# Performance work log

Hardware: AMD Instinct MI355X
Metric: run time of the kernel (lower is better)

## Reference

```python
import jax, jax.numpy as jnp
import numpy as np

T, B, D, H, L = 512, 128, 400, 400, 3


def setup_inputs() -> dict:
    key = jax.random.key(0)
    ks = jax.random.split(key, 12)
    x = jax.random.normal(ks[0], (T, B, D), dtype=jnp.float32)
    lengths = jnp.sort(jax.random.randint(ks[1], (B,), 1, T + 1))[::-1]
    s = 1.0 / np.sqrt(H)
    def w(k, shape):
        return jax.random.normal(k, shape, dtype=jnp.float32) * s
    return {
        "x": x,
        "lengths": lengths,
        # forward-direction cells: layer0 input D, layers 1..2 input 2H
        "Wih_f0": w(ks[2], (4 * H, D)),
        "Wih_f12": w(ks[3], (L - 1, 4 * H, 2 * H)),
        "Whh_f": w(ks[4], (L, 4 * H, H)),
        "b_f": jnp.zeros((L, 4 * H), jnp.float32),
        # backward-direction cells
        "Wih_b0": w(ks[5], (4 * H, D)),
        "Wih_b12": w(ks[6], (L - 1, 4 * H, 2 * H)),
        "Whh_b": w(ks[7], (L, 4 * H, H)),
        "b_b": jnp.zeros((L, 4 * H), jnp.float32),
    }


def _layer(x, mask, Wih, Whh, bias, reverse):
    # x: [T,B,Din], mask: [T,B] bool. Precompute input-side gates once.
    gx = jnp.einsum("tbd,gd->tbg", x, Wih) + bias  # [T,B,4H]
    nb, h_dim = x.shape[1], Whh.shape[-1]

    def step(carry, inp):
        h, c = carry
        g_x, m = inp
        g = g_x + h @ Whh.T
        i, f, gc, o = jnp.split(g, 4, axis=-1)
        i, f, o = jax.nn.sigmoid(i), jax.nn.sigmoid(f), jax.nn.sigmoid(o)
        gc = jnp.tanh(gc)
        c_new = f * c + i * gc
        h_new = o * jnp.tanh(c_new)
        m = m[:, None]
        # inactive sequences keep old state (fwd) / init zeros (bwd) -- matches packed semantics
        h = jnp.where(m, h_new, h)
        c = jnp.where(m, c_new, c)
        return (h, c), h

    if reverse:
        gx, m_seq = gx[::-1], mask[::-1]
    else:
        m_seq = mask
    init = (jnp.zeros((nb, h_dim), x.dtype), jnp.zeros((nb, h_dim), x.dtype))
    _, out = jax.lax.scan(step, init, (gx, m_seq))
    if reverse:
        out = out[::-1]
    return out * mask[:, :, None]


def reference(x, lengths, Wih_f0, Wih_f12, Whh_f, b_f, Wih_b0, Wih_b12, Whh_b, b_b):
    mask = jnp.arange(x.shape[0])[:, None] < lengths[None, :]  # [T,B]
    Wih_fs = [Wih_f0, Wih_f12[0], Wih_f12[1]]
    Wih_bs = [Wih_b0, Wih_b12[0], Wih_b12[1]]
    for l in range(L):
        f = _layer(x, mask, Wih_fs[l], Whh_f[l], b_f[l], reverse=False)
        b = _layer(x, mask, Wih_bs[l], Whh_b[l], b_b[l], reverse=True)
        x = jnp.concatenate([f, b], axis=-1)  # [T,B,2H]
    return x
```

## Files before the change

### kernel.cpp

```cpp
#include <hip/hip_runtime.h>
#include <stdint.h>
#include <stddef.h>

#define T_ 512
#define B_ 128
#define D_ 400
#define H_ 400
#define HP 416
#define GP 1664
#define NW 3328
#define K0P 448
#define K12P 832
#define NTILES 13
#define NGRP 8
#define REC_BLOCKS 208
#define PAIRS 208

#define GC_FSTRIDE 576

#define HBT_U64   ((size_t)16*2*16*PAIRS)
#define HBT_BYTES (HBT_U64*8)

#define WHHR_US8  ((size_t)2*13*4*2*13*64)
#define WHHR_BYTES (WHHR_US8*8*2)

typedef __attribute__((ext_vector_type(8))) __bf16 bf16x8;
typedef __attribute__((ext_vector_type(4))) float f32x4;
typedef __attribute__((ext_vector_type(8))) unsigned short us8;

__device__ __forceinline__ unsigned short f2bf(float f){
  unsigned u = __builtin_bit_cast(unsigned, f);
  u = (u + 0x7FFFu + ((u >> 16) & 1u)) >> 16;
  return (unsigned short)u;
}
__device__ __forceinline__ float bf2f(unsigned short s){
  unsigned u = ((unsigned)s) << 16;
  return __builtin_bit_cast(float, u);
}
__device__ __forceinline__ float sigm(float x){ return 1.f / (1.f + __expf(-x)); }
__device__ __forceinline__ float tanh_f(float x){
  float ax = fabsf(x);
  float e = __expf(-2.f * ax);
  float t = (1.f - e) / (1.f + e);
  return x < 0.f ? -t : t;
}
__device__ __forceinline__ void store_gx(float* p, float v){ *p = v; }
__device__ __forceinline__ void store_gx(unsigned short* p, float v){ *p = f2bf(v); }

__device__ __forceinline__ void h_store_u64(unsigned long long* p, unsigned long long v){
  __hip_atomic_store(p, v, __ATOMIC_RELAXED, __HIP_MEMORY_SCOPE_AGENT);
}
__device__ __forceinline__ unsigned long long h_load_u64(const unsigned long long* p){
  return __hip_atomic_load(p, __ATOMIC_RELAXED, __HIP_MEMORY_SCOPE_AGENT);
}

__device__ __forceinline__ void gl_lds16(const unsigned short* g, unsigned short* l){
  __builtin_amdgcn_global_load_lds(
      (const __attribute__((address_space(1))) unsigned int*)g,
      (__attribute__((address_space(3))) unsigned int*)l, 16, 0, 0);
}

__global__ void k_conv_x0(const float* __restrict__ x, unsigned short* __restrict__ xa){
  const size_t i = (size_t)blockIdx.x*256 + threadIdx.x;
  if (i >= (size_t)T_*B_*K0P) return;
  const int k = (int)(i % K0P);
  const size_t tb = i / K0P;
  xa[i] = f2bf(k < D_ ? x[tb*D_ + k] : 0.f);
}

__global__ void k_prep_wih(const float* __restrict__ wf, const float* __restrict__ wb,
                           int K, int mode, unsigned short* __restrict__ dst){
  const size_t i = (size_t)blockIdx.x*256 + threadIdx.x;
  if (i >= (size_t)NW*K) return;
  const int k = (int)(i % K);
  const int n = (int)(i / K);
  const int d = n / GP, ng = n % GP, g = ng / HP, r = ng % HP;
  const float* Wsrc = d ? wb : wf;
  float v = 0.f;
  if (r < H_){
    if (mode == 0){
      if (k < D_) v = Wsrc[(size_t)(g*H_ + r)*D_ + k];
    } else {
      int ks = (k < 400) ? k : ((k >= 416 && k < 816) ? (k - 16) : -1);
      if (ks >= 0) v = Wsrc[(size_t)(g*H_ + r)*800 + ks];
    }
  }
  dst[i] = f2bf(v);
}

__global__ void k_prep_whhR(const float* __restrict__ wf, const float* __restrict__ wb,
                            unsigned short* __restrict__ dst){
  const size_t i = (size_t)blockIdx.x*256 + threadIdx.x;
  if (i >= WHHR_US8) return;
  const int lane = (int)(i & 63);
  size_t q = i >> 6;
  const int kk = (int)(q % 13); q /= 13;
  const int ch = (int)(q % 2);  q /= 2;
  const int w  = (int)(q % 4);  q /= 4;
  const int tile = (int)(q % 13);
  const int dirx = (int)(q / 13);
  const int c  = tile*32 + ch*16 + (lane & 15);
  const int k0 = kk*32 + (lane >> 4)*8;
  const float* W = dirx ? wb : wf;
  unsigned short v[8];
  #pragma unroll
  for (int e = 0; e < 8; ++e){
    const int k = k0 + e;
    const float x = (c < H_ && k < H_) ? W[(size_t)(w*H_ + c)*H_ + k] : 0.f;
    v[e] = f2bf(x);
  }
  *(us8*)(dst + i*8) = *(const us8*)v;
}

__global__ void k_prep_bias(const float* __restrict__ bsf, const float* __restrict__ bsb,
                            float* __restrict__ dst){
  const int n = blockIdx.x*256 + threadIdx.x;
  if (n >= NW) return;
  const int d = n / GP, ng = n % GP, g = ng / HP, r = ng % HP;
  dst[n] = (r < H_) ? (d ? bsb : bsf)[g*H_ + r] : 0.f;
}

template<typename GXT>
__global__ __launch_bounds__(256) void gemm_gx(
    const unsigned short* __restrict__ X, int lda, int K,
    const unsigned short* __restrict__ W,
    const float* __restrict__ bias,
    GXT* __restrict__ gx,
    const int* __restrict__ lens)
{
  const int t = blockIdx.y;
  if (t >= lens[0]) return;
  const int n0 = blockIdx.x * 128;
  __shared__ unsigned short As[128*64];
  __shared__ unsigned short Bs[128*64];
  const int tid = threadIdx.x;
  const int l = tid & 63;
  const int w = tid >> 6;
  const int wm = (w >> 1) * 64, wn = (w & 1) * 64;
  const int lr = l & 15, lk = l >> 4;
  f32x4 acc[4][4];
  #pragma unroll
  for (int i = 0; i < 4; ++i)
    #pragma unroll
    for (int j = 0; j < 4; ++j) acc[i][j] = (f32x4){0.f,0.f,0.f,0.f};

  const unsigned short* Xb = X + (size_t)t * B_ * lda;
  const int srow = l >> 3, scol = (l & 7) * 8;

  for (int k0 = 0; k0 < K; k0 += 64){
    #pragma unroll
    for (int c = 0; c < 4; ++c){
      const int rb = w*32 + c*8;
      gl_lds16(Xb + (size_t)(rb + srow)*lda + k0 + scol, &As[rb*64]);
      gl_lds16(W  + (size_t)(n0 + rb + srow)*K  + k0 + scol, &Bs[rb*64]);
    }
    __syncthreads();
    #pragma unroll
    for (int kk = 0; kk < 2; ++kk){
      bf16x8 af[4], bfr[4];
      #pragma unroll
      for (int mi = 0; mi < 4; ++mi)
        af[mi] = __builtin_bit_cast(bf16x8, *(const us8*)&As[(wm + mi*16 + lr)*64 + kk*32 + lk*8]);
      #pragma unroll
      for (int ni = 0; ni < 4; ++ni)
        bfr[ni] = __builtin_bit_cast(bf16x8, *(const us8*)&Bs[(wn + ni*16 + lr)*64 + kk*32 + lk*8]);
      #pragma unroll
      for (int mi = 0; mi < 4; ++mi)
        #pragma unroll
        for (int ni = 0; ni < 4; ++ni)
          acc[mi][ni] = __builtin_amdgcn_mfma_f32_16x16x32_bf16(af[mi], bfr[ni], acc[mi][ni], 0, 0, 0);
    }
    __syncthreads();
  }
  #pragma unroll
  for (int ni = 0; ni < 4; ++ni){
    const int col = n0 + wn + ni*16 + lr;
    const float bv = bias[col];
    #pragma unroll
    for (int mi = 0; mi < 4; ++mi){
      #pragma unroll
      for (int r = 0; r < 4; ++r){
        const int b = wm + mi*16 + lk*4 + r;
        store_gx(gx + ((size_t)t*B_ + b)*NW + col, acc[mi][ni][r] + bv);
      }
    }
  }
}

template<typename GXT, bool LAST>
__global__ __launch_bounds__(256, 1) void lstm_rec(
    const GXT* __restrict__ gx,
    const unsigned short* __restrict__ whhR,
    const int* __restrict__ lens,
    unsigned long long* hbt,
    unsigned short* __restrict__ xn,
    float* __restrict__ out)
{
  __shared__ unsigned short HS[16*424];
  __shared__ float GC[4*GC_FSTRIDE];
  __shared__ float GXS[16*132];

  const int tid = threadIdx.x;
  const int bid = blockIdx.x;
  const int dir  = bid / 104;
  const int rem  = bid % 104;
  const int grp  = rem / NTILES;
  const int tile = rem % NTILES;
  const int l  = tid & 63;
  const int w  = tid >> 6;
  const int lr = l & 15;
  const int lk = l >> 4;
  const int cid = dir*NGRP + grp;

  us8 Bf0[13], Bf1[13];
  {
    const unsigned short* bs =
        whhR + ((size_t)((dir*13 + tile)*4 + w)*2*13*64 + l)*8;
    #pragma unroll
    for (int kk = 0; kk < 13; ++kk)
      Bf0[kk] = *(const us8*)(bs + (size_t)kk*512);
    const unsigned short* bs1 = bs + (size_t)13*64*8;
    #pragma unroll
    for (int kk = 0; kk < 13; ++kk)
      Bf1[kk] = *(const us8*)(bs1 + (size_t)kk*512);
  }
  const int grp_len = lens[grp*16];
  const int eb  = tid & 15;
  const int p2  = tid >> 4;
  const int mylen = lens[grp*16 + eb];
  float cs0 = 0.f, cs1 = 0.f, hs0 = 0.f, hs1 = 0.f;
  __syncthreads();

  int s_a = 0;
  const int pb = tid >> 4, q = tid & 15, qg = q >> 2, qj = (q & 3) * 8;
  unsigned long long* const myslot =
      hbt + (((size_t)cid*2)*16 + eb)*PAIRS + tile*16 + p2;

  for (int s = 0; s < T_; ++s){
    const int t = dir ? (T_ - 1 - s) : s;
    if (t >= grp_len) continue;

    f32x4 pfa, pfb;
    {
      const size_t goff = ((size_t)t*B_ + grp*16 + pb) * NW + (size_t)dir*GP + qg*HP + tile*32 + qj;
      if constexpr (sizeof(GXT) == 4){
        const float* gp = (const float*)gx + goff;
        pfa = *(const f32x4*)gp;
        pfb = *(const f32x4*)(gp + 4);
      } else {
        us8 v = *(const us8*)((const unsigned short*)gx + goff);
        pfa = (f32x4){bf2f(v[0]), bf2f(v[1]), bf2f(v[2]), bf2f(v[3])};
        pfb = (f32x4){bf2f(v[4]), bf2f(v[5]), bf2f(v[6]), bf2f(v[7])};
      }
    }

    {
      const unsigned rtag = (unsigned)s_a;
      const unsigned long long* hb =
          hbt + ((size_t)(cid*2 + (s_a & 1))*16)*PAIRS;
      unsigned long long v[13];
      #pragma unroll
      for (int j = 0; j < 13; ++j)
        v[j] = h_load_u64(hb + j*256 + tid);
      unsigned stale = 0;
      #pragma unroll
      for (int j = 0; j < 13; ++j)
        if ((unsigned)(v[j] >> 32) != rtag) stale |= 1u << j;
      while (stale){
        const unsigned m = stale;
        #pragma unroll
        for (int j = 0; j < 13; ++j)
          if (m & (1u << j)) v[j] = h_load_u64(hb + j*256 + tid);
        #pragma unroll
        for (int j = 0; j < 13; ++j)
          if ((m & (1u << j)) && (unsigned)(v[j] >> 32) == rtag) stale &= ~(1u << j);
      }
      #pragma unroll
      for (int j = 0; j < 13; ++j){
        const int idx = j*256 + tid;
        const int b = idx / PAIRS, p = idx % PAIRS;
        *(unsigned*)&HS[b*424 + 2*p] = (unsigned)v[j];
      }
    }
    __syncthreads();

    f32x4 a0 = (f32x4){0.f,0.f,0.f,0.f}, a1 = (f32x4){0.f,0.f,0.f,0.f};
    {
      const int ab = lr*424 + lk*8;
      #pragma unroll
      for (int kk = 0; kk < 13; ++kk){
        bf16x8 av = __builtin_bit_cast(bf16x8, *(const us8*)&HS[ab + kk*32]);
        a0 = __builtin_amdgcn_mfma_f32_16x16x32_bf16(av, Bf0[kk], a0, 0, 0, 0);
        a1 = __builtin_amdgcn_mfma_f32_16x16x32_bf16(av, Bf1[kk], a1, 0, 0, 0);
      }
    }
    {
      float* Gw = GC + w * GC_FSTRIDE;
      #pragma unroll
      for (int r = 0; r < 4; ++r){
        Gw[(lk*4 + r)*36 + lr]      = a0[r];
        Gw[(lk*4 + r)*36 + 16 + lr] = a1[r];
      }
      float* gp = GXS + pb*132 + qg*32 + qj;
      *(f32x4*)gp = pfa;
      *(f32x4*)(gp + 4) = pfb;
    }
    __syncthreads();

    const bool act = t < mylen;
    const int c0 = 2*p2, c1 = 2*p2 + 1;
    {
      const float gi0 = GC[0*GC_FSTRIDE + eb*36 + c0] + GXS[eb*132 + c0];
      const float gf0 = GC[1*GC_FSTRIDE + eb*36 + c0] + GXS[eb*132 + 32 + c0];
      const float gg0 = GC[2*GC_FSTRIDE + eb*36 + c0] + GXS[eb*132 + 64 + c0];
      const float go0 = GC[3*GC_FSTRIDE + eb*36 + c0] + GXS[eb*132 + 96 + c0];
      const float gi1 = GC[0*GC_FSTRIDE + eb*36 + c1] + GXS[eb*132 + c1];
      const float gf1 = GC[1*GC_FSTRIDE + eb*36 + c1] + GXS[eb*132 + 32 + c1];
      const float gg1 = GC[2*GC_FSTRIDE + eb*36 + c1] + GXS[eb*132 + 64 + c1];
      const float go1 = GC[3*GC_FSTRIDE + eb*36 + c1] + GXS[eb*132 + 96 + c1];
      const float cn0 = sigm(gf0)*cs0 + sigm(gi0)*tanh_f(gg0);
      const float hn0 = sigm(go0) * tanh_f(cn0);
      const float cn1 = sigm(gf1)*cs1 + sigm(gi1)*tanh_f(gg1);
      const float hn1 = sigm(go1) * tanh_f(cn1);
      if (act){ cs0 = cn0; hs0 = hn0; cs1 = cn1; hs1 = hn1; }
    }
    {
      const unsigned hu = (unsigned)f2bf(hs0) | ((unsigned)f2bf(hs1) << 16);
      const unsigned long long hv =
          (unsigned long long)hu | ((unsigned long long)(unsigned)(s_a + 1) << 32);
      h_store_u64(myslot + ((size_t)((s_a + 1) & 1))*16*PAIRS, hv);
    }
    if (act){
      const int bg = grp*16 + eb;
      const int hc = tile*32 + c0;
      if constexpr (LAST){
        float* op = out + ((size_t)t*B_ + bg)*800 + dir*H_ + hc;
        if (hc < H_)     op[0] = hs0;
        if (hc + 1 < H_) op[1] = hs1;
      } else {
        const unsigned hu = (unsigned)f2bf(hs0) | ((unsigned)f2bf(hs1) << 16);
        *(unsigned*)(xn + ((size_t)t*B_ + bg)*832 + (size_t)dir*HP + hc) = hu;
      }
    }
    ++s_a;
  }
}

template<typename GXT>
static void run_all(void* const* din, float* out, char* ws, hipStream_t stream)
{
  const float* x      = (const float*)din[0];
  const int* lens     = (const int*)din[1];
  const float* wihf0  = (const float*)din[2];
  const float* wihf12 = (const float*)din[3];
  const float* whhf   = (const float*)din[4];
  const float* bsf    = (const float*)din[5];
  const float* wihb0  = (const float*)din[6];
  const float* wihb12 = (const float*)din[7];
  const float* whhb   = (const float*)din[8];
  const float* bsb    = (const float*)din[9];

  char* p = ws;
  auto alloc = [&](size_t n){ char* r = p; p += (n + 255) & ~(size_t)255; return r; };
  GXT* gx            = (GXT*)alloc((size_t)T_*B_*NW*sizeof(GXT));
  unsigned short* xA = (unsigned short*)alloc((size_t)T_*B_*832*2);
  unsigned short* xB = (unsigned short*)alloc((size_t)T_*B_*832*2);
  unsigned short* wihp = (unsigned short*)alloc((size_t)NW*K12P*2);
  unsigned short* whhR = (unsigned short*)alloc(WHHR_BYTES);
  float* biasp       = (float*)alloc((size_t)NW*4);
  unsigned long long* hbt = (unsigned long long*)alloc(HBT_BYTES);

  hipMemsetAsync(out, 0, (size_t)T_*B_*800*4, stream);
  {
    size_t n = (size_t)T_*B_*K0P;
    k_conv_x0<<<dim3((unsigned)((n+255)/256)), dim3(256), 0, stream>>>(x, xA);
  }

  const unsigned short* xin[3] = {xA, xB, xA};
  unsigned short* xout[3] = {xB, xA, nullptr};
  const int ldas[3] = {K0P, 832, 832};
  const int Ks[3]   = {K0P, K12P, K12P};

  for (int lyr = 0; lyr < 3; ++lyr){
    const float* wf = (lyr == 0) ? wihf0 : wihf12 + (size_t)(lyr-1)*1600*800;
    const float* wb = (lyr == 0) ? wihb0 : wihb12 + (size_t)(lyr-1)*1600*800;
    {
      size_t n = (size_t)NW*Ks[lyr];
      k_prep_wih<<<dim3((unsigned)((n+255)/256)), dim3(256), 0, stream>>>(
          wf, wb, Ks[lyr], lyr ? 1 : 0, wihp);
    }
    k_prep_bias<<<dim3((NW+255)/256), dim3(256), 0, stream>>>(
        bsf + (size_t)lyr*1600, bsb + (size_t)lyr*1600, biasp);
    gemm_gx<GXT><<<dim3(26, 512), dim3(256), 0, stream>>>(
        xin[lyr], ldas[lyr], Ks[lyr], wihp, biasp, gx, lens);
    {
      size_t n = WHHR_US8;
      k_prep_whhR<<<dim3((unsigned)((n+255)/256)), dim3(256), 0, stream>>>(
          whhf + (size_t)lyr*1600*400, whhb + (size_t)lyr*1600*400, whhR);
    }
    hipMemsetAsync(hbt, 0, HBT_BYTES, stream);

    if (lyr < 2)
      lstm_rec<GXT,false><<<dim3(REC_BLOCKS), dim3(256), 0, stream>>>(
          gx, whhR, lens, hbt, xout[lyr], out);
    else
      lstm_rec<GXT,true><<<dim3(REC_BLOCKS), dim3(256), 0, stream>>>(
          gx, whhR, lens, hbt, nullptr, out);
  }
}

extern "C" void kernel_launch(void* const* d_in, const int* in_sizes, int n_in,
                              void* d_out, int out_size, void* d_ws, size_t ws_size,
                              hipStream_t stream)
{
  (void)in_sizes; (void)n_in; (void)out_size;
  auto align = [](size_t n){ return (n + 255) & ~(size_t)255; };
  const size_t fixed =
      align((size_t)T_*B_*832*2) * 2 +
      align((size_t)NW*K12P*2) +
      align(WHHR_BYTES) +
      align((size_t)NW*4) +
      align(HBT_BYTES);
  const size_t need32 = align((size_t)T_*B_*NW*4) + fixed;
  const size_t need16 = align((size_t)T_*B_*NW*2) + fixed;

  if (ws_size >= need32)
    run_all<float>(d_in, (float*)d_out, (char*)d_ws, stream);
  else if (ws_size >= need16)
    run_all<unsigned short>(d_in, (float*)d_out, (char*)d_ws, stream);
  else
    hipMemsetAsync(d_out, 0, (size_t)T_*B_*800*4, stream);
}
```

Measured before the change: 6.327 ms.

## Fuse input-projection GEMM into recurrent LSTM kernel with register-resident Wih

Removes the separate gx GEMM and its large T*B*4H intermediate buffer. Each recurrent block now keeps its slice of Wih in registers (26 k-chunks per gate pair), stages the x row for the current timestep into LDS, and does the input projection with MFMA inside every step before adding the recurrent term. The aim is to cut the gx write/read traffic and the extra launch. In exchange, the serial critical path of each step now carries twice the MFMA work plus an x load, and register pressure rises sharply (52 extra us8 fragments), which risks spills. Layer 0 input is also padded to 832 columns.

```diff
diff --git a/kernel.cpp b/kernel.cpp
--- a/kernel.cpp
+++ b/kernel.cpp
@@ -9,8 +9,7 @@
 #define HP 416
 #define GP 1664
 #define NW 3328
-#define K0P 448
-#define K12P 832
+#define KXP 832
 #define NTILES 13
 #define NGRP 8
 #define REC_BLOCKS 208
@@ -23,6 +22,8 @@
 
 #define WHHR_US8  ((size_t)2*13*4*2*13*64)
 #define WHHR_BYTES (WHHR_US8*8*2)
+#define WIHR_US8  ((size_t)2*13*4*2*26*64)
+#define WIHR_BYTES (WIHR_US8*8*2)
 
 typedef __attribute__((ext_vector_type(8))) __bf16 bf16x8;
 typedef __attribute__((ext_vector_type(4))) float f32x4;
@@ -44,8 +45,6 @@
   float t = (1.f - e) / (1.f + e);
   return x < 0.f ? -t : t;
 }
-__device__ __forceinline__ void store_gx(float* p, float v){ *p = v; }
-__device__ __forceinline__ void store_gx(unsigned short* p, float v){ *p = f2bf(v); }
 
 __device__ __forceinline__ void h_store_u64(unsigned long long* p, unsigned long long v){
   __hip_atomic_store(p, v, __ATOMIC_RELAXED, __HIP_MEMORY_SCOPE_AGENT);
@@ -54,38 +53,40 @@
   return __hip_atomic_load(p, __ATOMIC_RELAXED, __HIP_MEMORY_SCOPE_AGENT);
 }
 
-__device__ __forceinline__ void gl_lds16(const unsigned short* g, unsigned short* l){
-  __builtin_amdgcn_global_load_lds(
-      (const __attribute__((address_space(1))) unsigned int*)g,
-      (__attribute__((address_space(3))) unsigned int*)l, 16, 0, 0);
-}
-
 __global__ void k_conv_x0(const float* __restrict__ x, unsigned short* __restrict__ xa){
   const size_t i = (size_t)blockIdx.x*256 + threadIdx.x;
-  if (i >= (size_t)T_*B_*K0P) return;
-  const int k = (int)(i % K0P);
-  const size_t tb = i / K0P;
+  if (i >= (size_t)T_*B_*KXP) return;
+  const int k = (int)(i % KXP);
+  const size_t tb = i / KXP;
   xa[i] = f2bf(k < D_ ? x[tb*D_ + k] : 0.f);
 }
 
-__global__ void k_prep_wih(const float* __restrict__ wf, const float* __restrict__ wb,
-                           int K, int mode, unsigned short* __restrict__ dst){
+__global__ void k_prep_wihR(const float* __restrict__ wf, const float* __restrict__ wb,
+                            int mode, unsigned short* __restrict__ dst){
   const size_t i = (size_t)blockIdx.x*256 + threadIdx.x;
-  if (i >= (size_t)NW*K) return;
-  const int k = (int)(i % K);
-  const int n = (int)(i / K);
-  const int d = n / GP, ng = n % GP, g = ng / HP, r = ng % HP;
-  const float* Wsrc = d ? wb : wf;
-  float v = 0.f;
-  if (r < H_){
-    if (mode == 0){
-      if (k < D_) v = Wsrc[(size_t)(g*H_ + r)*D_ + k];
-    } else {
-      int ks = (k < 400) ? k : ((k >= 416 && k < 816) ? (k - 16) : -1);
-      if (ks >= 0) v = Wsrc[(size_t)(g*H_ + r)*800 + ks];
-    }
-  }
-  dst[i] = f2bf(v);
+  if (i >= WIHR_US8) return;
+  const int lane = (int)(i & 63);
+  size_t q = i >> 6;
+  const int kk = (int)(q % 26); q /= 26;
+  const int ch = (int)(q % 2);  q /= 2;
+  const int g  = (int)(q % 4);  q /= 4;
+  const int tile = (int)(q % 13);
+  const int dirx = (int)(q / 13);
+  const int c  = tile*32 + ch*16 + (lane & 15);
+  const int k0 = kk*32 + (lane >> 4)*8;
+  const float* W = dirx ? wb : wf;
+  const int stride = mode ? 800 : D_;
+  unsigned short v[8];
+  #pragma unroll
+  for (int e = 0; e < 8; ++e){
+    const int k = k0 + e;
+    int ks;
+    if (mode == 0) ks = (k < D_) ? k : -1;
+    else           ks = (k < 400) ? k : ((k >= 416 && k < 816) ? (k - 16) : -1);
+    const float x = (c < H_ && ks >= 0) ? W[(size_t)(g*H_ + c)*stride + ks] : 0.f;
+    v[e] = f2bf(x);
+  }
+  *(us8*)(dst + i*8) = *(const us8*)v;
 }
 
 __global__ void k_prep_whhR(const float* __restrict__ wf, const float* __restrict__ wb,
@@ -120,85 +121,20 @@
   dst[n] = (r < H_) ? (d ? bsb : bsf)[g*H_ + r] : 0.f;
 }
 
-template<typename GXT>
-__global__ __launch_bounds__(256) void gemm_gx(
-    const unsigned short* __restrict__ X, int lda, int K,
-    const unsigned short* __restrict__ W,
-    const float* __restrict__ bias,
-    GXT* __restrict__ gx,
-    const int* __restrict__ lens)
-{
-  const int t = blockIdx.y;
-  if (t >= lens[0]) return;
-  const int n0 = blockIdx.x * 128;
-  __shared__ unsigned short As[128*64];
-  __shared__ unsigned short Bs[128*64];
-  const int tid = threadIdx.x;
-  const int l = tid & 63;
-  const int w = tid >> 6;
-  const int wm = (w >> 1) * 64, wn = (w & 1) * 64;
-  const int lr = l & 15, lk = l >> 4;
-  f32x4 acc[4][4];
-  #pragma unroll
-  for (int i = 0; i < 4; ++i)
-    #pragma unroll
-    for (int j = 0; j < 4; ++j) acc[i][j] = (f32x4){0.f,0.f,0.f,0.f};
-
-  const unsigned short* Xb = X + (size_t)t * B_ * lda;
-  const int srow = l >> 3, scol = (l & 7) * 8;
-
-  for (int k0 = 0; k0 < K; k0 += 64){
-    #pragma unroll
-    for (int c = 0; c < 4; ++c){
-      const int rb = w*32 + c*8;
-      gl_lds16(Xb + (size_t)(rb + srow)*lda + k0 + scol, &As[rb*64]);
-      gl_lds16(W  + (size_t)(n0 + rb + srow)*K  + k0 + scol, &Bs[rb*64]);
-    }
-    __syncthreads();
-    #pragma unroll
-    for (int kk = 0; kk < 2; ++kk){
-      bf16x8 af[4], bfr[4];
-      #pragma unroll
-      for (int mi = 0; mi < 4; ++mi)
-        af[mi] = __builtin_bit_cast(bf16x8, *(const us8*)&As[(wm + mi*16 + lr)*64 + kk*32 + lk*8]);
-      #pragma unroll
-      for (int ni = 0; ni < 4; ++ni)
-        bfr[ni] = __builtin_bit_cast(bf16x8, *(const us8*)&Bs[(wn + ni*16 + lr)*64 + kk*32 + lk*8]);
-      #pragma unroll
-      for (int mi = 0; mi < 4; ++mi)
-        #pragma unroll
-        for (int ni = 0; ni < 4; ++ni)
-          acc[mi][ni] = __builtin_amdgcn_mfma_f32_16x16x32_bf16(af[mi], bfr[ni], acc[mi][ni], 0, 0, 0);
-    }
-    __syncthreads();
-  }
-  #pragma unroll
-  for (int ni = 0; ni < 4; ++ni){
-    const int col = n0 + wn + ni*16 + lr;
-    const float bv = bias[col];
-    #pragma unroll
-    for (int mi = 0; mi < 4; ++mi){
-      #pragma unroll
-      for (int r = 0; r < 4; ++r){
-        const int b = wm + mi*16 + lk*4 + r;
-        store_gx(gx + ((size_t)t*B_ + b)*NW + col, acc[mi][ni][r] + bv);
-      }
-    }
-  }
-}
-
-template<typename GXT, bool LAST>
+template<bool LAST>
 __global__ __launch_bounds__(256, 1) void lstm_rec(
-    const GXT* __restrict__ gx,
+    const unsigned short* __restrict__ xin,
+    const unsigned short* __restrict__ wihR,
     const unsigned short* __restrict__ whhR,
+    const float* __restrict__ biasp,
     const int* __restrict__ lens,
     unsigned long long* hbt,
     unsigned short* __restrict__ xn,
     float* __restrict__ out)
 {
   __shared__ unsigned short HS[16*424];
+  __shared__ unsigned short XS[16*840];
   __shared__ float GC[4*GC_FSTRIDE];
-  __shared__ float GXS[16*132];
 
   const int tid = threadIdx.x;
   const int bid = blockIdx.x;
@@ -224,15 +160,34 @@
     for (int kk = 0; kk < 13; ++kk)
       Bf1[kk] = *(const us8*)(bs1 + (size_t)kk*512);
   }
+  us8 Wf0[26], Wf1[26];
+  {
+    const unsigned short* ws0 =
+        wihR + ((size_t)(((dir*13 + tile)*4 + w)*2 + 0)*26*64 + l)*8;
+    #pragma unroll
+    for (int kk = 0; kk < 26; ++kk)
+      Wf0[kk] = *(const us8*)(ws0 + (size_t)kk*512);
+    const unsigned short* ws1 = ws0 + (size_t)26*64*8;
+    #pragma unroll
+    for (int kk = 0; kk < 26; ++kk)
+      Wf1[kk] = *(const us8*)(ws1 + (size_t)kk*512);
+  }
+
   const int grp_len = lens[grp*16];
   const int eb  = tid & 15;
   const int p2  = tid >> 4;
   const int mylen = lens[grp*16 + eb];
+  const int c0 = 2*p2, c1 = 2*p2 + 1;
+  float b0g[4], b1g[4];
+  #pragma unroll
+  for (int g = 0; g < 4; ++g){
+    b0g[g] = biasp[dir*GP + g*HP + tile*32 + c0];
+    b1g[g] = biasp[dir*GP + g*HP + tile*32 + c1];
+  }
   float cs0 = 0.f, cs1 = 0.f, hs0 = 0.f, hs1 = 0.f;
   __syncthreads();
 
   int s_a = 0;
-  const int pb = tid >> 4, q = tid & 15, qg = q >> 2, qj = (q & 3) * 8;
   unsigned long long* const myslot =
       hbt + (((size_t)cid*2)*16 + eb)*PAIRS + tile*16 + p2;
 
@@ -240,20 +195,17 @@
     const int t = dir ? (T_ - 1 - s) : s;
     if (t >= grp_len) continue;
 
-    f32x4 pfa, pfb;
-    {
-      const size_t goff = ((size_t)t*B_ + grp*16 + pb) * NW + (size_t)dir*GP + qg*HP + tile*32 + qj;
-      if constexpr (sizeof(GXT) == 4){
-        const float* gp = (const float*)gx + goff;
-        pfa = *(const f32x4*)gp;
-        pfb = *(const f32x4*)(gp + 4);
-      } else {
-        us8 v = *(const us8*)((const unsigned short*)gx + goff);
-        pfa = (f32x4){bf2f(v[0]), bf2f(v[1]), bf2f(v[2]), bf2f(v[3])};
-        pfb = (f32x4){bf2f(v[4]), bf2f(v[5]), bf2f(v[6]), bf2f(v[7])};
-      }
-    }
-
+    unsigned long long vx[13];
+    {
+      const unsigned long long* xrow =
+          (const unsigned long long*)(xin + ((size_t)t*B_ + grp*16)*KXP);
+      #pragma unroll
+      for (int j = 0; j < 13; ++j){
+        const int idx = j*256 + tid;
+        const int b = idx / 208, qq = idx % 208;
+        vx[j] = xrow[(size_t)b*208 + qq];
+      }
+    }
     {
       const unsigned rtag = (unsigned)s_a;
       const unsigned long long* hb =
@@ -282,10 +234,23 @@
         *(unsigned*)&HS[b*424 + 2*p] = (unsigned)v[j];
       }
     }
+    #pragma unroll
+    for (int j = 0; j < 13; ++j){
+      const int idx = j*256 + tid;
+      const int b = idx / 208, qq = idx % 208;
+      *(unsigned long long*)&XS[b*840 + qq*4] = vx[j];
+    }
     __syncthreads();
 
     f32x4 a0 = (f32x4){0.f,0.f,0.f,0.f}, a1 = (f32x4){0.f,0.f,0.f,0.f};
     {
+      const int abx = lr*840 + lk*8;
+      #pragma unroll
+      for (int kk = 0; kk < 26; ++kk){
+        bf16x8 xa = __builtin_bit_cast(bf16x8, *(const us8*)&XS[abx + kk*32]);
+        a0 = __builtin_amdgcn_mfma_f32_16x16x32_bf16(xa, Wf0[kk], a0, 0, 0, 0);
+        a1 = __builtin_amdgcn_mfma_f32_16x16x32_bf16(xa, Wf1[kk], a1, 0, 0, 0);
+      }
       const int ab = lr*424 + lk*8;
       #pragma unroll
       for (int kk = 0; kk < 13; ++kk){
@@ -301,23 +266,19 @@
         Gw[(lk*4 + r)*36 + lr]      = a0[r];
         Gw[(lk*4 + r)*36 + 16 + lr] = a1[r];
       }
-      float* gp = GXS + pb*132 + qg*32 + qj;
-      *(f32x4*)gp = pfa;
-      *(f32x4*)(gp + 4) = pfb;
     }
     __syncthreads();
 
     const bool act = t < mylen;
-    const int c0 = 2*p2, c1 = 2*p2 + 1;
-    {
-      const float gi0 = GC[0*GC_FSTRIDE + eb*36 + c0] + GXS[eb*132 + c0];
-      const float gf0 = GC[1*GC_FSTRIDE + eb*36 + c0] + GXS[eb*132 + 32 + c0];
-      const float gg0 = GC[2*GC_FSTRIDE + eb*36 + c0] + GXS[eb*132 + 64 + c0];
-      const float go0 = GC[3*GC_FSTRIDE + eb*36 + c0] + GXS[eb*132 + 96 + c0];
-      const float gi1 = GC[0*GC_FSTRIDE + eb*36 + c1] + GXS[eb*132 + c1];
-      const float gf1 = GC[1*GC_FSTRIDE + eb*36 + c1] + GXS[eb*132 + 32 + c1];
-      const float gg1 = GC[2*GC_FSTRIDE + eb*36 + c1] + GXS[eb*132 + 64 + c1];
-      const float go1 = GC[3*GC_FSTRIDE + eb*36 + c1] + GXS[eb*132 + 96 + c1];
+    {
+      const float gi0 = GC[0*GC_FSTRIDE + eb*36 + c0] + b0g[0];
+      const float gf0 = GC[1*GC_FSTRIDE + eb*36 + c0] + b0g[1];
+      const float gg0 = GC[2*GC_FSTRIDE + eb*36 + c0] + b0g[2];
+      const float go0 = GC[3*GC_FSTRIDE + eb*36 + c0] + b0g[3];
+      const float gi1 = GC[0*GC_FSTRIDE + eb*36 + c1] + b1g[0];
+      const float gf1 = GC[1*GC_FSTRIDE + eb*36 + c1] + b1g[1];
+      const float gg1 = GC[2*GC_FSTRIDE + eb*36 + c1] + b1g[2];
+      const float go1 = GC[3*GC_FSTRIDE + eb*36 + c1] + b1g[3];
       const float cn0 = sigm(gf0)*cs0 + sigm(gi0)*tanh_f(gg0);
       const float hn0 = sigm(go0) * tanh_f(cn0);
       const float cn1 = sigm(gf1)*cs1 + sigm(gi1)*tanh_f(gg1);
@@ -339,14 +300,13 @@
         if (hc + 1 < H_) op[1] = hs1;
       } else {
         const unsigned hu = (unsigned)f2bf(hs0) | ((unsigned)f2bf(hs1) << 16);
-        *(unsigned*)(xn + ((size_t)t*B_ + bg)*832 + (size_t)dir*HP + hc) = hu;
+        *(unsigned*)(xn + ((size_t)t*B_ + bg)*KXP + (size_t)dir*HP + hc) = hu;
       }
     }
     ++s_a;
   }
 }
 
-template<typename GXT>
 static void run_all(void* const* din, float* out, char* ws, hipStream_t stream)
 {
   const float* x      = (const float*)din[0];
@@ -362,37 +322,32 @@
 
   char* p = ws;
   auto alloc = [&](size_t n){ char* r = p; p += (n + 255) & ~(size_t)255; return r; };
-  GXT* gx            = (GXT*)alloc((size_t)T_*B_*NW*sizeof(GXT));
-  unsigned short* xA = (unsigned short*)alloc((size_t)T_*B_*832*2);
-  unsigned short* xB = (unsigned short*)alloc((size_t)T_*B_*832*2);
-  unsigned short* wihp = (unsigned short*)alloc((size_t)NW*K12P*2);
+  unsigned short* xA = (unsigned short*)alloc((size_t)T_*B_*KXP*2);
+  unsigned short* xB = (unsigned short*)alloc((size_t)T_*B_*KXP*2);
+  unsigned short* wihR = (unsigned short*)alloc(WIHR_BYTES);
   unsigned short* whhR = (unsigned short*)alloc(WHHR_BYTES);
   float* biasp       = (float*)alloc((size_t)NW*4);
   unsigned long long* hbt = (unsigned long long*)alloc(HBT_BYTES);
 
   hipMemsetAsync(out, 0, (size_t)T_*B_*800*4, stream);
   {
-    size_t n = (size_t)T_*B_*K0P;
+    size_t n = (size_t)T_*B_*KXP;
     k_conv_x0<<<dim3((unsigned)((n+255)/256)), dim3(256), 0, stream>>>(x, xA);
   }
 
-  const unsigned short* xin[3] = {xA, xB, xA};
-  unsigned short* xout[3] = {xB, xA, nullptr};
-  const int ldas[3] = {K0P, 832, 832};
-  const int Ks[3]   = {K0P, K12P, K12P};
+  const unsigned short* xinv[3] = {xA, xB, xA};
+  unsigned short* xoutv[3] = {xB, xA, nullptr};
 
   for (int lyr = 0; lyr < 3; ++lyr){
     const float* wf = (lyr == 0) ? wihf0 : wihf12 + (size_t)(lyr-1)*1600*800;
     const float* wb = (lyr == 0) ? wihb0 : wihb12 + (size_t)(lyr-1)*1600*800;
     {
-      size_t n = (size_t)NW*Ks[lyr];
-      k_prep_wih<<<dim3((unsigned)((n+255)/256)), dim3(256), 0, stream>>>(
-          wf, wb, Ks[lyr], lyr ? 1 : 0, wihp);
+      size_t n = WIHR_US8;
+      k_prep_wihR<<<dim3((unsigned)((n+255)/256)), dim3(256), 0, stream>>>(
+          wf, wb, lyr ? 1 : 0, wihR);
     }
     k_prep_bias<<<dim3((NW+255)/256), dim3(256), 0, stream>>>(
         bsf + (size_t)lyr*1600, bsb + (size_t)lyr*1600, biasp);
-    gemm_gx<GXT><<<dim3(26, 512), dim3(256), 0, stream>>>(
-        xin[lyr], ldas[lyr], Ks[lyr], wihp, biasp, gx, lens);
     {
       size_t n = WHHR_US8;
       k_prep_whhR<<<dim3((unsigned)((n+255)/256)), dim3(256), 0, stream>>>(
@@ -401,11 +356,11 @@
     hipMemsetAsync(hbt, 0, HBT_BYTES, stream);
 
     if (lyr < 2)
-      lstm_rec<GXT,false><<<dim3(REC_BLOCKS), dim3(256), 0, stream>>>(
-          gx, whhR, lens, hbt, xout[lyr], out);
+      lstm_rec<false><<<dim3(REC_BLOCKS), dim3(256), 0, stream>>>(
+          xinv[lyr], wihR, whhR, biasp, lens, hbt, xoutv[lyr], out);
     else
-      lstm_rec<GXT,true><<<dim3(REC_BLOCKS), dim3(256), 0, stream>>>(
-          gx, whhR, lens, hbt, nullptr, out);
+      lstm_rec<true><<<dim3(REC_BLOCKS), dim3(256), 0, stream>>>(
+          xinv[lyr], wihR, whhR, biasp, lens, hbt, nullptr, out);
   }
 }
 
@@ -415,19 +370,15 @@
 {
   (void)in_sizes; (void)n_in; (void)out_size;
   auto align = [](size_t n){ return (n + 255) & ~(size_t)255; };
-  const size_t fixed =
-      align((size_t)T_*B_*832*2) * 2 +
-      align((size_t)NW*K12P*2) +
+  const size_t need =
+      align((size_t)T_*B_*KXP*2) * 2 +
+      align(WIHR_BYTES) +
       align(WHHR_BYTES) +
       align((size_t)NW*4) +
       align(HBT_BYTES);
-  const size_t need32 = align((size_t)T_*B_*NW*4) + fixed;
-  const size_t need16 = align((size_t)T_*B_*NW*2) + fixed;
-
-  if (ws_size >= need32)
-    run_all<float>(d_in, (float*)d_out, (char*)d_ws, stream);
-  else if (ws_size >= need16)
-    run_all<unsigned short>(d_in, (float*)d_out, (char*)d_ws, stream);
+
+  if (ws_size >= need)
+    run_all(d_in, (float*)d_out, (char*)d_ws, stream);
   else
     hipMemsetAsync(d_out, 0, (size_t)T_*B_*800*4, stream);
 }
```

Result: faster. 5.593 ms (-11.6%).
